# Kernel tuning notes

Measured on AMD Instinct MI355X. Metric: run time of the kernel, lower is better.

The kernel has to match this reference:

```python
import jax, jax.numpy as jnp
import numpy as np

B, C, T = 8, 256, 2048
DS = 4
SC = C // DS          # tsa_scale = 64
DEPTH = 256           # temporal_depth (band width)
BN_EPS = 1e-5


def _conv_bn_relu(x, W, b, g, beta, mu, var):
    # 1x1 conv on [B, C, T, 1] layout == channel matmul, then eval-mode BN, then ReLU
    y = jnp.einsum('bctz,oc->botz', x, W) + b[None, :, None, None]
    inv = g / jnp.sqrt(var + BN_EPS)
    y = (y - mu[None, :, None, None]) * inv[None, :, None, None] + beta[None, :, None, None]
    return jax.nn.relu(y)


def setup_inputs() -> dict:
    key = jax.random.key(0)
    ks = jax.random.split(key, 20)
    inp = {"x": jax.random.normal(ks[0], (B, C, T, 1), jnp.float32)}
    for name, oc, base in (("k", SC, 1), ("q", SC, 7), ("v", C, 13)):
        inp[name + "W"] = jax.random.normal(ks[base], (oc, C), jnp.float32) * 0.05
        inp[name + "b"] = jax.random.normal(ks[base + 1], (oc,), jnp.float32) * 0.05
        inp[name + "g"] = 1.0 + 0.05 * jax.random.normal(ks[base + 2], (oc,), jnp.float32)
        inp[name + "beta"] = jax.random.normal(ks[base + 3], (oc,), jnp.float32) * 0.05
        inp[name + "mu"] = jax.random.normal(ks[base + 4], (oc,), jnp.float32) * 0.05
        inp[name + "var"] = 1.0 + 0.1 * jax.random.uniform(ks[base + 5], (oc,), jnp.float32)
    return inp


def reference(x, kW, kb, kg, kbeta, kmu, kvar,
              qW, qb, qg, qbeta, qmu, qvar,
              vW, vb, vg, vbeta, vmu, vvar):
    key = _conv_bn_relu(x, kW, kb, kg, kbeta, kmu, kvar)[..., 0]                      # [B, SC, T]
    query = _conv_bn_relu(x, qW, qb, qg, qbeta, qmu, qvar)[..., 0].transpose(0, 2, 1)  # [B, T, SC]
    value = _conv_bn_relu(x, vW, vb, vg, vbeta, vmu, vvar)[..., 0].transpose(0, 2, 1)  # [B, T, C]

    i = jnp.arange(T)
    # tril(diag=0) * triu(diag=-(DEPTH-1)): causal band of width DEPTH
    mask = ((i[:, None] >= i[None, :]) & (i[:, None] - i[None, :] <= DEPTH - 1)).astype(x.dtype)

    s = jnp.einsum('btd,bds->bts', query, key) * mask / np.float32(np.sqrt(SC))
    s = jnp.exp(s - jnp.max(s, axis=2, keepdims=True)) * mask
    # NOTE: original torch code does `torch.sum(...)[0]`, indexing batch 0 of the
    # sum tensor ([T,1]) and broadcasting it across the batch. Replicated faithfully.
    s = s / (jnp.sum(s, axis=2, keepdims=True)[0] + 1e-30)

    tsa_out = jnp.einsum('bts,bsc->btc', s, value)                                     # [B, T, C]
    return x + tsa_out.transpose(0, 2, 1)[..., None]                                   # res_skip
```

## Files before the change

### kernel.cpp

```cpp
#include <hip/hip_runtime.h>

#define TDIM 2048

typedef __bf16 bf16_t;
typedef bf16_t bf16x8 __attribute__((ext_vector_type(8)));
typedef float f32x4 __attribute__((ext_vector_type(4)));
typedef unsigned short us8 __attribute__((ext_vector_type(8)));

__device__ __forceinline__ unsigned short f2bf(float x) {
  unsigned u = __builtin_bit_cast(unsigned, x);
  u += 0x7fffu + ((u >> 16) & 1u);
  return (unsigned short)(u >> 16);
}

__global__ __launch_bounds__(256) void k_qkv(
    const float* __restrict__ x,
    const float* __restrict__ kW, const float* __restrict__ kb,
    const float* __restrict__ kg, const float* __restrict__ kbe,
    const float* __restrict__ kmu, const float* __restrict__ kva,
    const float* __restrict__ qW, const float* __restrict__ qb,
    const float* __restrict__ qg, const float* __restrict__ qbe,
    const float* __restrict__ qmu, const float* __restrict__ qva,
    const float* __restrict__ vW, const float* __restrict__ vb,
    const float* __restrict__ vg, const float* __restrict__ vbe,
    const float* __restrict__ vmu, const float* __restrict__ vva,
    unsigned short* __restrict__ vv,
    unsigned short* __restrict__ kT,
    unsigned short* __restrict__ qT)
{
  const int tb  = blockIdx.x;
  const int gid = blockIdx.y;
  const int b   = blockIdx.z;
  const int tid = threadIdx.x;
  const int lane = tid & 63, wv = tid >> 6;
  const int m = lane & 15, quad = lane >> 4;
  const int t0 = tb * 64;

  __shared__ unsigned short Ws[128 * 136];
  __shared__ unsigned short Xs[64 * 72];
  __shared__ float invs[128];
  __shared__ float effbs[128];

  if (tid < 128) {
    int G = gid * 128 + tid;
    float gg = (G < 64) ? kg[G]  : (G < 128) ? qg[G - 64]  : vg[G - 128];
    float vvv= (G < 64) ? kva[G] : (G < 128) ? qva[G - 64] : vva[G - 128];
    float bb = (G < 64) ? kb[G]  : (G < 128) ? qb[G - 64]  : vb[G - 128];
    float mm = (G < 64) ? kmu[G] : (G < 128) ? qmu[G - 64] : vmu[G - 128];
    float be = (G < 64) ? kbe[G] : (G < 128) ? qbe[G - 64] : vbe[G - 128];
    float inv = gg * rsqrtf(vvv + 1e-5f);
    invs[tid]  = inv;
    effbs[tid] = (bb - mm) * inv + be;
  }
  __syncthreads();

  const f32x4 fz = {0.f, 0.f, 0.f, 0.f};
  f32x4 acc[2][4];
#pragma unroll
  for (int i = 0; i < 2; ++i)
#pragma unroll
    for (int j = 0; j < 4; ++j) acc[i][j] = fz;

  for (int ch = 0; ch < 2; ++ch) {
    __syncthreads();
#pragma unroll 4
    for (int it = 0; it < 16; ++it) {
      int idx = it * 256 + tid;
      int row = idx >> 5;
      int c4  = (idx & 31) * 4;
      int G = gid * 128 + row;
      const float* Wp = (G < 64) ? (kW + G * 256)
                       : (G < 128) ? (qW + (G - 64) * 256)
                                   : (vW + (G - 128) * 256);
      float4 w4 = *(const float4*)(Wp + ch * 128 + c4);
      float inv = invs[row];
      ushort4 s4;
      s4.x = f2bf(w4.x * inv); s4.y = f2bf(w4.y * inv);
      s4.z = f2bf(w4.z * inv); s4.w = f2bf(w4.w * inv);
      *(ushort4*)&Ws[row * 136 + c4] = s4;
    }
    for (int cx = 0; cx < 2; ++cx) {
      __syncthreads();
      {
        int t  = tid & 63;
        int cb = b * 256 + ch * 128 + cx * 64;
#pragma unroll 4
        for (int i = 0; i < 16; ++i) {
          int c = i * 4 + (tid >> 6);
          float v = x[(size_t)(cb + c) * TDIM + t0 + t];
          int csw = (((c >> 3) ^ (t >> 3)) << 3) | (c & 7);
          Xs[t * 72 + csw] = f2bf(v);
        }
      }
      __syncthreads();
#pragma unroll
      for (int kk = 0; kk < 2; ++kk) {
        bf16x8 af[2];
#pragma unroll
        for (int mt = 0; mt < 2; ++mt) {
          int row = wv * 32 + mt * 16 + m;
          af[mt] = *(const bf16x8*)&Ws[row * 136 + cx * 64 + kk * 32 + quad * 8];
        }
#pragma unroll
        for (int nt = 0; nt < 4; ++nt) {
          int t = nt * 16 + m;
          int blk = (kk * 4 + quad) ^ (t >> 3);
          bf16x8 bfr = *(const bf16x8*)&Xs[t * 72 + blk * 8];
          acc[0][nt] = __builtin_amdgcn_mfma_f32_16x16x32_bf16(af[0], bfr, acc[0][nt], 0, 0, 0);
          acc[1][nt] = __builtin_amdgcn_mfma_f32_16x16x32_bf16(af[1], bfr, acc[1][nt], 0, 0, 0);
        }
      }
    }
  }
  if (gid == 0) {
#pragma unroll
    for (int mt = 0; mt < 2; ++mt)
#pragma unroll
      for (int nt = 0; nt < 4; ++nt) {
        int ocl = wv * 32 + mt * 16 + quad * 4;
        int t = t0 + nt * 16 + m;
        ushort4 s4;
        float y0 = fmaxf(acc[mt][nt][0] + effbs[ocl + 0], 0.f);
        float y1 = fmaxf(acc[mt][nt][1] + effbs[ocl + 1], 0.f);
        float y2 = fmaxf(acc[mt][nt][2] + effbs[ocl + 2], 0.f);
        float y3 = fmaxf(acc[mt][nt][3] + effbs[ocl + 3], 0.f);
        s4.x = f2bf(y0); s4.y = f2bf(y1); s4.z = f2bf(y2); s4.w = f2bf(y3);
        unsigned short* dst = (ocl < 64)
            ? (kT + ((size_t)(b * TDIM + t)) * 64 + ocl)
            : (qT + ((size_t)(b * TDIM + t)) * 64 + (ocl - 64));
        *(ushort4*)dst = s4;
      }
  } else {
#pragma unroll
    for (int mt = 0; mt < 2; ++mt)
#pragma unroll
      for (int nt = 0; nt < 4; ++nt)
#pragma unroll
        for (int r = 0; r < 4; ++r) {
          int ocl = wv * 32 + mt * 16 + quad * 4 + r;
          float y = fmaxf(acc[mt][nt][r] + effbs[ocl], 0.f);
          int c = (gid - 1) * 128 + ocl;
          int t = t0 + nt * 16 + m;
          vv[(size_t)(b * 256 + c) * TDIM + t] = f2bf(y);
        }
  }
}

__global__ __launch_bounds__(512, 1) void k_denom(
    const unsigned short* __restrict__ kT,
    const unsigned short* __restrict__ qT,
    float* __restrict__ denom0)
{
  const int t0d = blockIdx.x * 16;
  const int tid = threadIdx.x;
  const int lane = tid & 63, w = tid >> 6;
  const int m = lane & 15, quad = lane >> 4;

  __shared__ unsigned short Qs[16 * 64];
  __shared__ unsigned short Ks[272 * 64];
  __shared__ float pmaxs[8][16];
  __shared__ float psums[8][16];

  {
    const unsigned short* qg = qT + (size_t)t0d * 64;
#pragma unroll
    for (int it = 0; it < 5; ++it) {
      int idx = it * 512 + tid;
      if (idx < 2304) {
        int row = idx >> 3, dblk = idx & 7;
        us8 v = {0, 0, 0, 0, 0, 0, 0, 0};
        if (row < 16) {
          v = *(const us8*)(qg + row * 64 + dblk * 8);
          *(us8*)&Qs[row * 64 + ((dblk ^ (row & 7)) << 3)] = v;
        } else {
          int s = row - 16;
          int sg = t0d - 256 + s;
          if (sg >= 0) v = *(const us8*)(kT + (size_t)sg * 64 + dblk * 8);
          *(us8*)&Ks[s * 64 + ((dblk ^ (s & 7)) << 3)] = v;
        }
      }
    }
  }
  __syncthreads();

  const int jn = (w == 0) ? 3 : 2;
  f32x4 sc[3];
  {
    int t = m;
    bf16x8 qf0 = *(const bf16x8*)&Qs[t * 64 + ((quad ^ (t & 7)) << 3)];
    bf16x8 qf1 = *(const bf16x8*)&Qs[t * 64 + (((4 + quad) ^ (t & 7)) << 3)];
    const f32x4 fz = {0.f, 0.f, 0.f, 0.f};
#pragma unroll
    for (int jj = 0; jj < 3; ++jj) {
      if (jj < jn) {
        int j = w + jj * 8;
        int sr = 16 * j + m;
        f32x4 a = fz;
        bf16x8 kf0 = *(const bf16x8*)&Ks[sr * 64 + ((quad ^ (sr & 7)) << 3)];
        a = __builtin_amdgcn_mfma_f32_16x16x32_bf16(qf0, kf0, a, 0, 0, 0);
        bf16x8 kf1 = *(const bf16x8*)&Ks[sr * 64 + (((4 + quad) ^ (sr & 7)) << 3)];
        a = __builtin_amdgcn_mfma_f32_16x16x32_bf16(qf1, kf1, a, 0, 0, 0);
        sc[jj] = a;
      }
    }
  }

  float mx[4] = {0.f, 0.f, 0.f, 0.f};
#pragma unroll
  for (int jj = 0; jj < 3; ++jj)
    if (jj < jn) {
      int j = w + jj * 8;
#pragma unroll
      for (int r = 0; r < 4; ++r) {
        float v = sc[jj][r] * 0.125f;
        sc[jj][r] = v;
        int tg = t0d + quad * 4 + r;
        int sg = t0d - 256 + 16 * j + m;
        if (sg >= 0 && sg <= tg && tg - sg < 256) mx[r] = fmaxf(mx[r], v);
      }
    }
#pragma unroll
  for (int d = 1; d < 16; d <<= 1)
#pragma unroll
    for (int r = 0; r < 4; ++r) mx[r] = fmaxf(mx[r], __shfl_xor(mx[r], d, 64));
  if (m == 0)
#pragma unroll
    for (int r = 0; r < 4; ++r) pmaxs[w][quad * 4 + r] = mx[r];
  __syncthreads();

  float mxf[4];
#pragma unroll
  for (int r = 0; r < 4; ++r) {
    float v = pmaxs[0][quad * 4 + r];
#pragma unroll
    for (int ww = 1; ww < 8; ++ww) v = fmaxf(v, pmaxs[ww][quad * 4 + r]);
    mxf[r] = v;
  }
  float sm[4] = {0.f, 0.f, 0.f, 0.f};
#pragma unroll
  for (int jj = 0; jj < 3; ++jj)
    if (jj < jn) {
      int j = w + jj * 8;
#pragma unroll
      for (int r = 0; r < 4; ++r) {
        int tg = t0d + quad * 4 + r;
        int sg = t0d - 256 + 16 * j + m;
        if (sg >= 0 && sg <= tg && tg - sg < 256) sm[r] += __expf(sc[jj][r] - mxf[r]);
      }
    }
#pragma unroll
  for (int d = 1; d < 16; d <<= 1)
#pragma unroll
    for (int r = 0; r < 4; ++r) sm[r] += __shfl_xor(sm[r], d, 64);
  if (m == 0)
#pragma unroll
    for (int r = 0; r < 4; ++r) psums[w][quad * 4 + r] = sm[r];
  __syncthreads();

  if (tid < 16) {
    float s = 0.f;
#pragma unroll
    for (int ww = 0; ww < 8; ++ww) s += psums[ww][tid];
    denom0[t0d + tid] = s;
  }
}

__global__ __launch_bounds__(512, 4) void k_attn(
    const float* __restrict__ x,
    const unsigned short* __restrict__ vv,
    const unsigned short* __restrict__ kT,
    const unsigned short* __restrict__ qT,
    const float* __restrict__ denom0,
    float* __restrict__ out)
{
  const int tb = blockIdx.x, ch = blockIdx.y, b = blockIdx.z;
  const int tid = threadIdx.x;
  const int lane = tid & 63, w = tid >> 6;
  const int m = lane & 15, quad = lane >> 4;
  const int t0 = tb * 64;

  __shared__ unsigned short SM[27136];
  __shared__ float pmaxs[128];
  unsigned short* Qs = SM;
  unsigned short* Ks = SM + 4096;
  unsigned short* Ps = SM;
  unsigned short* Vs = SM + 22016;

  {
    const unsigned short* qg  = qT + ((size_t)b * TDIM + t0) * 64;
    const unsigned short* kgb = kT + (size_t)b * TDIM * 64;
#pragma unroll
    for (int it = 0; it < 6; ++it) {
      int idx = it * 512 + tid;
      int row = idx >> 3, dblk = idx & 7;
      us8 v = {0, 0, 0, 0, 0, 0, 0, 0};
      if (row < 64) {
        v = *(const us8*)(qg + row * 64 + dblk * 8);
        *(us8*)&Qs[row * 64 + ((dblk ^ (row & 7)) << 3)] = v;
      } else {
        int s = row - 64;
        int sg = t0 - 256 + s;
        if (sg >= 0) v = *(const us8*)(kgb + (size_t)sg * 64 + dblk * 8);
        *(us8*)&Ks[s * 64 + ((dblk ^ (s & 7)) << 3)] = v;
      }
    }
  }
  __syncthreads();

  const int rt = w & 3, half = w >> 2;
  const int j0 = half ? 9 : 0;
  const int jn = half ? 8 : 9;
  f32x4 sc[9];
  {
    int t = rt * 16 + m;
    bf16x8 qf0 = *(const bf16x8*)&Qs[t * 64 + ((quad ^ (t & 7)) << 3)];
    bf16x8 qf1 = *(const bf16x8*)&Qs[t * 64 + (((4 + quad) ^ (t & 7)) << 3)];
    const f32x4 fz = {0.f, 0.f, 0.f, 0.f};
#pragma unroll
    for (int jj = 0; jj < 9; ++jj) {
      if (jj < jn) {
        int sr = 16 * (rt + j0 + jj) + m;
        f32x4 a = fz;
        bf16x8 kf0 = *(const bf16x8*)&Ks[sr * 64 + ((quad ^ (sr & 7)) << 3)];
        a = __builtin_amdgcn_mfma_f32_16x16x32_bf16(qf0, kf0, a, 0, 0, 0);
        bf16x8 kf1 = *(const bf16x8*)&Ks[sr * 64 + (((4 + quad) ^ (sr & 7)) << 3)];
        a = __builtin_amdgcn_mfma_f32_16x16x32_bf16(qf1, kf1, a, 0, 0, 0);
        sc[jj] = a;
      }
    }
  }

  const int tw = t0 + rt * 16;
  float mx[4] = {0.f, 0.f, 0.f, 0.f};
#pragma unroll
  for (int jj = 0; jj < 9; ++jj)
    if (jj < jn) {
#pragma unroll
      for (int r = 0; r < 4; ++r) {
        float v = sc[jj][r] * 0.125f;
        sc[jj][r] = v;
        int tg = tw + quad * 4 + r;
        int sg = t0 - 256 + 16 * (rt + j0 + jj) + m;
        if (sg >= 0 && sg <= tg && tg - sg < 256) mx[r] = fmaxf(mx[r], v);
      }
    }
#pragma unroll
  for (int d = 1; d < 16; d <<= 1)
#pragma unroll
    for (int r = 0; r < 4; ++r) mx[r] = fmaxf(mx[r], __shfl_xor(mx[r], d, 64));
  if (m == 0)
#pragma unroll
    for (int r = 0; r < 4; ++r) pmaxs[half * 64 + rt * 16 + quad * 4 + r] = mx[r];

  float dval[4];
#pragma unroll
  for (int r = 0; r < 4; ++r) dval[r] = denom0[tw + quad * 4 + r];

  __syncthreads();

  {
    us8 z = {0, 0, 0, 0, 0, 0, 0, 0};
#pragma unroll
    for (int it = 0; it < 6; ++it) {
      int idx = it * 512 + tid;
      if (idx < 2752) *(us8*)&Ps[idx * 8] = z;
    }
  }
  float mxf[4], rden[4];
#pragma unroll
  for (int r = 0; r < 4; ++r) {
    int row = rt * 16 + quad * 4 + r;
    mxf[r] = fmaxf(pmaxs[row], pmaxs[64 + row]);
    rden[r] = 1.f / (dval[r] + 1e-30f);
  }
#pragma unroll
  for (int jj = 0; jj < 9; ++jj)
    if (jj < jn) {
#pragma unroll
      for (int r = 0; r < 4; ++r) {
        int tg = tw + quad * 4 + r;
        int sg = t0 - 256 + 16 * (rt + j0 + jj) + m;
        bool ib = (sg >= 0 && sg <= tg && tg - sg < 256);
        sc[jj][r] = ib ? __expf(sc[jj][r] - mxf[r]) * rden[r] : 0.f;
      }
    }
  __syncthreads();

#pragma unroll
  for (int jj = 0; jj < 9; ++jj)
    if (jj < jn) {
      int col = 16 * (rt + j0 + jj) + m;
#pragma unroll
      for (int r = 0; r < 4; ++r)
        Ps[(rt * 16 + quad * 4 + r) * 344 + col] = f2bf(sc[jj][r]);
    }
  __syncthreads();

  const int cbase = ch * 128 + w * 16;
  unsigned short* Vsw = Vs + w * 640;
  const unsigned short* vg = vv + ((size_t)(b * 256 + cbase + (lane >> 2))) * TDIM;
  const int si = (lane & 3) * 8;
  const f32x4 fz = {0.f, 0.f, 0.f, 0.f};
  f32x4 acc[4] = {fz, fz, fz, fz};

  us8 vreg = {0, 0, 0, 0, 0, 0, 0, 0};
  {
    int sg = t0 - 256 + si;
    if (sg >= 0) vreg = *(const us8*)(vg + sg);
  }
#pragma unroll
  for (int chunk = 0; chunk < 10; ++chunk) {
    us8 vnext = {0, 0, 0, 0, 0, 0, 0, 0};
    if (chunk < 9) {
      int sg = t0 - 256 + (chunk + 1) * 32 + si;
      if (sg >= 0) vnext = *(const us8*)(vg + sg);
    }
    *(us8*)&Vsw[(lane >> 2) * 40 + si] = vreg;
    bf16x8 bfr = *(const bf16x8*)&Vsw[m * 40 + quad * 8];
#pragma unroll
    for (int mt = 0; mt < 4; ++mt) {
      bf16x8 af = *(const bf16x8*)&Ps[(mt * 16 + m) * 344 + chunk * 32 + quad * 8];
      acc[mt] = __builtin_amdgcn_mfma_f32_16x16x32_bf16(af, bfr, acc[mt], 0, 0, 0);
    }
    vreg = vnext;
  }

#pragma unroll
  for (int mt = 0; mt < 4; ++mt) {
    int c = cbase + m;
    int t = t0 + mt * 16 + quad * 4;
    size_t off = (size_t)(b * 256 + c) * TDIM + t;
    float4 xv = *(const float4*)(x + off);
    float4 o;
    o.x = xv.x + acc[mt][0];
    o.y = xv.y + acc[mt][1];
    o.z = xv.z + acc[mt][2];
    o.w = xv.w + acc[mt][3];
    *(float4*)(out + off) = o;
  }
}

extern "C" void kernel_launch(void* const* d_in, const int* in_sizes, int n_in,
                              void* d_out, int out_size, void* d_ws, size_t ws_size,
                              hipStream_t stream) {
  const float* x   = (const float*)d_in[0];
  const float* kW  = (const float*)d_in[1];
  const float* kb  = (const float*)d_in[2];
  const float* kg  = (const float*)d_in[3];
  const float* kbe = (const float*)d_in[4];
  const float* kmu = (const float*)d_in[5];
  const float* kva = (const float*)d_in[6];
  const float* qW  = (const float*)d_in[7];
  const float* qb  = (const float*)d_in[8];
  const float* qg  = (const float*)d_in[9];
  const float* qbe = (const float*)d_in[10];
  const float* qmu = (const float*)d_in[11];
  const float* qva = (const float*)d_in[12];
  const float* vW  = (const float*)d_in[13];
  const float* vb  = (const float*)d_in[14];
  const float* vg  = (const float*)d_in[15];
  const float* vbe = (const float*)d_in[16];
  const float* vmu = (const float*)d_in[17];
  const float* vva = (const float*)d_in[18];

  unsigned short* vv  = (unsigned short*)d_ws;
  unsigned short* kTp = vv + (size_t)8 * 256 * TDIM;
  unsigned short* qTp = kTp + (size_t)8 * TDIM * 64;
  float* denom0 = (float*)(qTp + (size_t)8 * TDIM * 64);
  float* outp = (float*)d_out;

  k_qkv<<<dim3(32, 3, 8), 256, 0, stream>>>(x,
      kW, kb, kg, kbe, kmu, kva,
      qW, qb, qg, qbe, qmu, qva,
      vW, vb, vg, vbe, vmu, vva, vv, kTp, qTp);
  k_denom<<<dim3(128), 512, 0, stream>>>(kTp, qTp, denom0);
  k_attn<<<dim3(32, 2, 8), 512, 0, stream>>>(x, vv, kTp, qTp, denom0, outp);
}
```

Measured before the change: 141.0 us.

## Add prep kernel for MFMA-fragment layouts; async LDS loads in QKV; direct V fragments

A new prep kernel converts x to bf16 and rearranges it, along with the BN-folded weights, into MFMA-fragment-ordered buffers, and computes the effective biases once. The QKV GEMM then double-buffers these tiles with global_load_lds and no longer converts or swizzles per block. In the attention kernel, V fragments are now loaded straight from global memory into registers instead of going through an LDS round-trip, which cuts shared memory use. The cost is an extra kernel launch plus an extra global write and read of a transposed bf16 copy of x.

```diff
diff --git a/kernel.cpp b/kernel.cpp
--- a/kernel.cpp
+++ b/kernel.cpp
@@ -13,7 +13,13 @@
   return (unsigned short)(u >> 16);
 }
 
-__global__ __launch_bounds__(256) void k_qkv(
+__device__ __forceinline__ void gl_lds16(const unsigned short* g, unsigned short* l) {
+  __builtin_amdgcn_global_load_lds(
+      (const __attribute__((address_space(1))) unsigned int*)g,
+      (__attribute__((address_space(3))) unsigned int*)l, 16, 0, 0);
+}
+
+__global__ __launch_bounds__(256) void k_prep(
     const float* __restrict__ x,
     const float* __restrict__ kW, const float* __restrict__ kb,
     const float* __restrict__ kg, const float* __restrict__ kbe,
@@ -24,35 +30,120 @@
     const float* __restrict__ vW, const float* __restrict__ vb,
     const float* __restrict__ vg, const float* __restrict__ vbe,
     const float* __restrict__ vmu, const float* __restrict__ vva,
+    unsigned short* __restrict__ xTf,
+    unsigned short* __restrict__ effWf,
+    float* __restrict__ effb)
+{
+  const int w = blockIdx.x;
+  const int tid = threadIdx.x;
+
+  if (w < 256) {
+    const int tb = w & 31, b = w >> 5;
+    const int t0 = tb * 64;
+    __shared__ float Lf[64][66];
+    for (int cc = 0; cc < 4; ++cc) {
+      if (cc) __syncthreads();
+#pragma unroll
+      for (int pass = 0; pass < 4; ++pass) {
+        int cl = pass * 16 + (tid >> 4);
+        int tp = (tid & 15) * 4;
+        float4 vx = *(const float4*)(x + (size_t)(b * 256 + cc * 64 + cl) * TDIM + t0 + tp);
+        Lf[cl][tp] = vx.x; Lf[cl][tp + 1] = vx.y;
+        Lf[cl][tp + 2] = vx.z; Lf[cl][tp + 3] = vx.w;
+      }
+      __syncthreads();
+      unsigned short* dst = xTf + (((size_t)(b * 32 + tb) * 4 + cc) * 512) * 8;
+#pragma unroll
+      for (int pass = 0; pass < 2; ++pass) {
+        int f = pass * 256 + tid;
+        int nt = f >> 7, cblk = (f >> 4) & 7, m = f & 15;
+        int t = nt * 16 + m;
+        ushort4 lo, hi;
+        lo.x = f2bf(Lf[cblk * 8 + 0][t]); lo.y = f2bf(Lf[cblk * 8 + 1][t]);
+        lo.z = f2bf(Lf[cblk * 8 + 2][t]); lo.w = f2bf(Lf[cblk * 8 + 3][t]);
+        hi.x = f2bf(Lf[cblk * 8 + 4][t]); hi.y = f2bf(Lf[cblk * 8 + 5][t]);
+        hi.z = f2bf(Lf[cblk * 8 + 6][t]); hi.w = f2bf(Lf[cblk * 8 + 7][t]);
+        *(ushort4*)(dst + f * 8) = lo;
+        *(ushort4*)(dst + f * 8 + 4) = hi;
+      }
+    }
+  } else {
+    const int idx = w - 256;
+    const int gid = idx >> 2, cc = idx & 3;
+    unsigned short* dst = effWf + (size_t)idx * 1024 * 8;
+#pragma unroll
+    for (int pass = 0; pass < 4; ++pass) {
+      int f = pass * 256 + tid;
+      int ocblk = f >> 7, cblk = (f >> 4) & 7, m = f & 15;
+      int G = gid * 128 + ocblk * 16 + m;
+      const float* Wp = (G < 64) ? (kW + G * 256)
+                       : (G < 128) ? (qW + (G - 64) * 256)
+                                   : (vW + (G - 128) * 256);
+      float gg = (G < 64) ? kg[G]  : (G < 128) ? qg[G - 64]  : vg[G - 128];
+      float vr = (G < 64) ? kva[G] : (G < 128) ? qva[G - 64] : vva[G - 128];
+      float inv = gg * rsqrtf(vr + 1e-5f);
+      int c = cc * 64 + cblk * 8;
+      float4 a = *(const float4*)(Wp + c);
+      float4 bq = *(const float4*)(Wp + c + 4);
+      ushort4 lo, hi;
+      lo.x = f2bf(a.x * inv);  lo.y = f2bf(a.y * inv);
+      lo.z = f2bf(a.z * inv);  lo.w = f2bf(a.w * inv);
+      hi.x = f2bf(bq.x * inv); hi.y = f2bf(bq.y * inv);
+      hi.z = f2bf(bq.z * inv); hi.w = f2bf(bq.w * inv);
+      *(ushort4*)(dst + f * 8) = lo;
+      *(ushort4*)(dst + f * 8 + 4) = hi;
+    }
+    if (idx == 0) {
+      for (int G = tid; G < 384; G += 256) {
+        float gg = (G < 64) ? kg[G]  : (G < 128) ? qg[G - 64]  : vg[G - 128];
+        float vr = (G < 64) ? kva[G] : (G < 128) ? qva[G - 64] : vva[G - 128];
+        float bb = (G < 64) ? kb[G]  : (G < 128) ? qb[G - 64]  : vb[G - 128];
+        float mm = (G < 64) ? kmu[G] : (G < 128) ? qmu[G - 64] : vmu[G - 128];
+        float be = (G < 64) ? kbe[G] : (G < 128) ? qbe[G - 64] : vbe[G - 128];
+        float inv = gg * rsqrtf(vr + 1e-5f);
+        effb[G] = (bb - mm) * inv + be;
+      }
+    }
+  }
+}
+
+__global__ __launch_bounds__(256, 3) void k_qkv(
+    const unsigned short* __restrict__ effWf,
+    const float* __restrict__ effb,
+    const unsigned short* __restrict__ xTf,
     unsigned short* __restrict__ vv,
     unsigned short* __restrict__ kT,
     unsigned short* __restrict__ qT)
 {
-  const int tb  = blockIdx.x;
-  const int gid = blockIdx.y;
-  const int b   = blockIdx.z;
+  const int tb = blockIdx.x, gid = blockIdx.y, b = blockIdx.z;
   const int tid = threadIdx.x;
   const int lane = tid & 63, wv = tid >> 6;
   const int m = lane & 15, quad = lane >> 4;
   const int t0 = tb * 64;
 
-  __shared__ unsigned short Ws[128 * 136];
-  __shared__ unsigned short Xs[64 * 72];
-  __shared__ float invs[128];
+  __shared__ unsigned short Wb[2][8192];
+  __shared__ unsigned short Xb[2][4096];
   __shared__ float effbs[128];
 
-  if (tid < 128) {
-    int G = gid * 128 + tid;
-    float gg = (G < 64) ? kg[G]  : (G < 128) ? qg[G - 64]  : vg[G - 128];
-    float vvv= (G < 64) ? kva[G] : (G < 128) ? qva[G - 64] : vva[G - 128];
-    float bb = (G < 64) ? kb[G]  : (G < 128) ? qb[G - 64]  : vb[G - 128];
-    float mm = (G < 64) ? kmu[G] : (G < 128) ? qmu[G - 64] : vmu[G - 128];
-    float be = (G < 64) ? kbe[G] : (G < 128) ? qbe[G - 64] : vbe[G - 128];
-    float inv = gg * rsqrtf(vvv + 1e-5f);
-    invs[tid]  = inv;
-    effbs[tid] = (bb - mm) * inv + be;
-  }
-  __syncthreads();
+  if (tid < 128) effbs[tid] = effb[gid * 128 + tid];
+
+  const unsigned short* wbase = effWf + (size_t)gid * 4 * 1024 * 8;
+  const unsigned short* xbase = xTf + ((size_t)(b * 32 + tb) * 4) * 512 * 8;
+
+  auto stage = [&](int cc, int bufi) {
+    const unsigned short* ws = wbase + (size_t)cc * 1024 * 8;
+    const unsigned short* xs = xbase + (size_t)cc * 512 * 8;
+#pragma unroll
+    for (int i = 0; i < 4; ++i) {
+      int ii = wv * 4 + i;
+      gl_lds16(ws + (ii * 64 + lane) * 8, &Wb[bufi][ii * 512]);
+    }
+#pragma unroll
+    for (int i = 0; i < 2; ++i) {
+      int ii = wv * 2 + i;
+      gl_lds16(xs + (ii * 64 + lane) * 8, &Xb[bufi][ii * 512]);
+    }
+  };
 
   const f32x4 fz = {0.f, 0.f, 0.f, 0.f};
   f32x4 acc[2][4];
@@ -61,57 +152,30 @@
 #pragma unroll
     for (int j = 0; j < 4; ++j) acc[i][j] = fz;
 
-  for (int ch = 0; ch < 2; ++ch) {
+  stage(0, 0);
+  for (int cc = 0; cc < 4; ++cc) {
     __syncthreads();
-#pragma unroll 4
-    for (int it = 0; it < 16; ++it) {
-      int idx = it * 256 + tid;
-      int row = idx >> 5;
-      int c4  = (idx & 31) * 4;
-      int G = gid * 128 + row;
-      const float* Wp = (G < 64) ? (kW + G * 256)
-                       : (G < 128) ? (qW + (G - 64) * 256)
-                                   : (vW + (G - 128) * 256);
-      float4 w4 = *(const float4*)(Wp + ch * 128 + c4);
-      float inv = invs[row];
-      ushort4 s4;
-      s4.x = f2bf(w4.x * inv); s4.y = f2bf(w4.y * inv);
-      s4.z = f2bf(w4.z * inv); s4.w = f2bf(w4.w * inv);
-      *(ushort4*)&Ws[row * 136 + c4] = s4;
-    }
-    for (int cx = 0; cx < 2; ++cx) {
-      __syncthreads();
-      {
-        int t  = tid & 63;
-        int cb = b * 256 + ch * 128 + cx * 64;
-#pragma unroll 4
-        for (int i = 0; i < 16; ++i) {
-          int c = i * 4 + (tid >> 6);
-          float v = x[(size_t)(cb + c) * TDIM + t0 + t];
-          int csw = (((c >> 3) ^ (t >> 3)) << 3) | (c & 7);
-          Xs[t * 72 + csw] = f2bf(v);
-        }
-      }
-      __syncthreads();
-#pragma unroll
-      for (int kk = 0; kk < 2; ++kk) {
-        bf16x8 af[2];
-#pragma unroll
-        for (int mt = 0; mt < 2; ++mt) {
-          int row = wv * 32 + mt * 16 + m;
-          af[mt] = *(const bf16x8*)&Ws[row * 136 + cx * 64 + kk * 32 + quad * 8];
-        }
-#pragma unroll
-        for (int nt = 0; nt < 4; ++nt) {
-          int t = nt * 16 + m;
-          int blk = (kk * 4 + quad) ^ (t >> 3);
-          bf16x8 bfr = *(const bf16x8*)&Xs[t * 72 + blk * 8];
-          acc[0][nt] = __builtin_amdgcn_mfma_f32_16x16x32_bf16(af[0], bfr, acc[0][nt], 0, 0, 0);
-          acc[1][nt] = __builtin_amdgcn_mfma_f32_16x16x32_bf16(af[1], bfr, acc[1][nt], 0, 0, 0);
-        }
-      }
-    }
-  }
+    if (cc < 3) stage(cc + 1, (cc + 1) & 1);
+    const unsigned short* Wc = Wb[cc & 1];
+    const unsigned short* Xc = Xb[cc & 1];
+#pragma unroll
+    for (int kk = 0; kk < 2; ++kk) {
+      int cb = kk * 4 + quad;
+      bf16x8 af[2], bfv[4];
+#pragma unroll
+      for (int mt = 0; mt < 2; ++mt)
+        af[mt] = *(const bf16x8*)&Wc[(((wv * 2 + mt) * 8 + cb) * 16 + m) * 8];
+#pragma unroll
+      for (int nt = 0; nt < 4; ++nt)
+        bfv[nt] = *(const bf16x8*)&Xc[((nt * 8 + cb) * 16 + m) * 8];
+#pragma unroll
+      for (int mt = 0; mt < 2; ++mt)
+#pragma unroll
+        for (int nt = 0; nt < 4; ++nt)
+          acc[mt][nt] = __builtin_amdgcn_mfma_f32_16x16x32_bf16(af[mt], bfv[nt], acc[mt][nt], 0, 0, 0);
+    }
+  }
+
   if (gid == 0) {
 #pragma unroll
     for (int mt = 0; mt < 2; ++mt)
@@ -120,11 +184,10 @@
         int ocl = wv * 32 + mt * 16 + quad * 4;
         int t = t0 + nt * 16 + m;
         ushort4 s4;
-        float y0 = fmaxf(acc[mt][nt][0] + effbs[ocl + 0], 0.f);
-        float y1 = fmaxf(acc[mt][nt][1] + effbs[ocl + 1], 0.f);
-        float y2 = fmaxf(acc[mt][nt][2] + effbs[ocl + 2], 0.f);
-        float y3 = fmaxf(acc[mt][nt][3] + effbs[ocl + 3], 0.f);
-        s4.x = f2bf(y0); s4.y = f2bf(y1); s4.z = f2bf(y2); s4.w = f2bf(y3);
+        s4.x = f2bf(fmaxf(acc[mt][nt][0] + effbs[ocl + 0], 0.f));
+        s4.y = f2bf(fmaxf(acc[mt][nt][1] + effbs[ocl + 1], 0.f));
+        s4.z = f2bf(fmaxf(acc[mt][nt][2] + effbs[ocl + 2], 0.f));
+        s4.w = f2bf(fmaxf(acc[mt][nt][3] + effbs[ocl + 3], 0.f));
         unsigned short* dst = (ocl < 64)
             ? (kT + ((size_t)(b * TDIM + t)) * 64 + ocl)
             : (qT + ((size_t)(b * TDIM + t)) * 64 + (ocl - 64));
@@ -279,12 +342,11 @@
   const int m = lane & 15, quad = lane >> 4;
   const int t0 = tb * 64;
 
-  __shared__ unsigned short SM[27136];
+  __shared__ unsigned short SM[24576];
   __shared__ float pmaxs[128];
   unsigned short* Qs = SM;
   unsigned short* Ks = SM + 4096;
   unsigned short* Ps = SM;
-  unsigned short* Vs = SM + 22016;
 
   {
     const unsigned short* qg  = qT + ((size_t)b * TDIM + t0) * 64;
@@ -397,26 +459,20 @@
   __syncthreads();
 
   const int cbase = ch * 128 + w * 16;
-  unsigned short* Vsw = Vs + w * 640;
-  const unsigned short* vg = vv + ((size_t)(b * 256 + cbase + (lane >> 2))) * TDIM;
-  const int si = (lane & 3) * 8;
+  const unsigned short* vrow = vv + (size_t)(b * 256 + cbase + m) * TDIM;
   const f32x4 fz = {0.f, 0.f, 0.f, 0.f};
   f32x4 acc[4] = {fz, fz, fz, fz};
 
   us8 vreg = {0, 0, 0, 0, 0, 0, 0, 0};
-  {
-    int sg = t0 - 256 + si;
-    if (sg >= 0) vreg = *(const us8*)(vg + sg);
-  }
+  if (t0 >= 256) vreg = *(const us8*)(vrow + t0 - 256 + quad * 8);
 #pragma unroll
   for (int chunk = 0; chunk < 10; ++chunk) {
     us8 vnext = {0, 0, 0, 0, 0, 0, 0, 0};
     if (chunk < 9) {
-      int sg = t0 - 256 + (chunk + 1) * 32 + si;
-      if (sg >= 0) vnext = *(const us8*)(vg + sg);
-    }
-    *(us8*)&Vsw[(lane >> 2) * 40 + si] = vreg;
-    bf16x8 bfr = *(const bf16x8*)&Vsw[m * 40 + quad * 8];
+      int sbase = t0 - 256 + (chunk + 1) * 32;
+      if (sbase >= 0) vnext = *(const us8*)(vrow + sbase + quad * 8);
+    }
+    bf16x8 bfr = __builtin_bit_cast(bf16x8, vreg);
 #pragma unroll
     for (int mt = 0; mt < 4; ++mt) {
       bf16x8 af = *(const bf16x8*)&Ps[(mt * 16 + m) * 344 + chunk * 32 + quad * 8];
@@ -467,12 +523,16 @@
   unsigned short* kTp = vv + (size_t)8 * 256 * TDIM;
   unsigned short* qTp = kTp + (size_t)8 * TDIM * 64;
   float* denom0 = (float*)(qTp + (size_t)8 * TDIM * 64);
+  unsigned short* xTf = (unsigned short*)(denom0 + 2048);
+  unsigned short* effWf = xTf + (size_t)8 * 256 * TDIM;
+  float* effb = (float*)(effWf + 384 * 256);
   float* outp = (float*)d_out;
 
-  k_qkv<<<dim3(32, 3, 8), 256, 0, stream>>>(x,
+  k_prep<<<dim3(268), 256, 0, stream>>>(x,
       kW, kb, kg, kbe, kmu, kva,
       qW, qb, qg, qbe, qmu, qva,
-      vW, vb, vg, vbe, vmu, vva, vv, kTp, qTp);
+      vW, vb, vg, vbe, vmu, vva, xTf, effWf, effb);
+  k_qkv<<<dim3(32, 3, 8), 256, 0, stream>>>(effWf, effb, xTf, vv, kTp, qTp);
   k_denom<<<dim3(128), 512, 0, stream>>>(kTp, qTp, denom0);
   k_attn<<<dim3(32, 2, 8), 512, 0, stream>>>(x, vv, kTp, qTp, denom0, outp);
 }
```

After: 135.8 us. 3.7% less time.
